# Performance work log

Hardware: AMD Instinct MI355X
Metric: run time of the kernel (lower is better)

## Reference

```python
import jax, jax.numpy as jnp
import numpy as np

N_HEADS = 16
B = 8
SEQ = 1024
HID = 1024
TOT = B * SEQ


def setup_inputs() -> dict:
    key = jax.random.key(0)
    k1, k2, k3 = jax.random.split(key, 3)
    hidden_states = jax.random.normal(k1, (TOT, HID), dtype=jnp.float32)
    Wqkv = jax.random.normal(k2, (3 * HID, HID), dtype=jnp.float32) * 0.02
    Bqkv = jax.random.normal(k3, (3 * HID,), dtype=jnp.float32) * 0.02
    cu_seqlens = (jnp.arange(B + 1, dtype=jnp.int32) * SEQ)
    return {"hidden_states": hidden_states, "Wqkv": Wqkv, "Bqkv": Bqkv,
            "cu_seqlens": cu_seqlens, "max_s": SEQ}


def reference(hidden_states, Wqkv, Bqkv, cu_seqlens, max_s):
    # qkv projection: F.linear(hidden, Wqkv, Bqkv) -> [T, 3H]
    T, H = hidden_states.shape
    h = N_HEADS
    d = H // h
    b = cu_seqlens.shape[0] - 1
    S = T // b  # equal-length packing; cu_seqlens = arange(b+1)*S
    qkv = hidden_states @ Wqkv.T + Bqkv                      # [T, 3H]
    qkv = qkv.reshape(b, S, 3, h, d)
    q, k, v = qkv[:, :, 0], qkv[:, :, 1], qkv[:, :, 2]       # [b, S, h, d]
    scale = 1.0 / jnp.sqrt(jnp.asarray(d, dtype=q.dtype))
    scores = jnp.einsum("bshd,bthd->bhst", q, k) * scale     # [b, h, S, S]
    probs = jax.nn.softmax(scores, axis=-1)                  # p_dropout = 0.0
    ctx = jnp.einsum("bhst,bthd->bshd", probs, v)            # [b, S, h, d]
    return ctx.reshape(T, H)
```

## Files before the change

### kernel.cpp

```cpp
#include <hip/hip_runtime.h>

typedef __attribute__((ext_vector_type(8))) __bf16 bf16x8;
typedef __attribute__((ext_vector_type(2))) __bf16 bf16x2;
typedef __attribute__((ext_vector_type(4))) float f32x4;
typedef __attribute__((ext_vector_type(4))) unsigned int u32x4;

#define AS1 __attribute__((address_space(1)))
#define AS3 __attribute__((address_space(3)))

__device__ __forceinline__ unsigned short f2b(float f) {
    union { float f; unsigned int u; } c; c.f = f;
    unsigned int r = c.u + 0x7fffu + ((c.u >> 16) & 1u);
    return (unsigned short)(r >> 16);
}

__device__ __forceinline__ unsigned int pack2(float a, float b) {
    bf16x2 t;
    t[0] = (__bf16)a;
    t[1] = (__bf16)b;
    return __builtin_bit_cast(unsigned int, t);
}

__device__ __forceinline__ void gload_lds16(const void* g, void* l) {
    __builtin_amdgcn_global_load_lds((const AS1 unsigned int*)g,
                                     (AS3 unsigned int*)l, 16, 0, 0);
}

__global__ void cvt2_kernel(const float* __restrict__ in0,
                            unsigned short* __restrict__ out0, int n0,
                            const float* __restrict__ in1,
                            unsigned short* __restrict__ out1, int n1) {
    int i = blockIdx.x * blockDim.x + threadIdx.x;
    int stride = gridDim.x * blockDim.x;
    const int nt = n0 + n1;
    for (; i < nt; i += stride) {
        if (i < n0) {
            float4 v = reinterpret_cast<const float4*>(in0)[i];
            ushort4 o;
            o.x = f2b(v.x); o.y = f2b(v.y); o.z = f2b(v.z); o.w = f2b(v.w);
            reinterpret_cast<ushort4*>(out0)[i] = o;
        } else {
            const int j = i - n0;
            const int E = j * 4;
            const int row = E >> 10;
            const int col = E & 1023;
            float4 v = reinterpret_cast<const float4*>(in1)[j];
            ushort4 o;
            o.x = f2b(v.x); o.y = f2b(v.y); o.z = f2b(v.z); o.w = f2b(v.w);
            const int kt = col >> 5, kg = (col >> 3) & 3, e = col & 7;
            const int n16 = row >> 4, fr = row & 15;
            const size_t oaddr = ((size_t)(kt * 192 + n16) << 9)
                               + ((kg * 16 + fr) << 3) + e;
            *reinterpret_cast<ushort4*>(out1 + oaddr) = o;
        }
    }
}

__global__ __launch_bounds__(512, 4) void qkv_gemm(
    const unsigned short* __restrict__ A,
    const unsigned short* __restrict__ Bw,
    const float* __restrict__ bias,
    unsigned short* __restrict__ qb,
    unsigned short* __restrict__ kb,
    unsigned short* __restrict__ vb)
{
    __shared__ __align__(16) char smem[49152];
    const int tid = threadIdx.x;
    const int lane = tid & 63, w = tid >> 6;
    const int wm = w >> 1, wn = w & 1;
    const int wg = (blockIdx.x & 7) * 96 + (blockIdx.x >> 3);
    const int mt = wg / 24;
    const int nt = wg % 24;
    const int fr = lane & 15, kg = lane >> 4;

    const int sr = lane >> 2;
    const int g  = (lane & 3) ^ ((sr >> 1) & 3);
    const unsigned short* a_srcg = A + (size_t)(mt * 256 + w * 16 + sr) * 1024 + g * 8;
    const unsigned short* bfp = Bw + (((size_t)(nt * 8 + wn * 4)) << 9) + lane * 8;

    f32x4 acc[4][4] = {};
    const int pg = (kg ^ ((fr >> 1) & 3)) * 16;
    const int aoffA = (wm * 64 + fr) * 64;

#define STAGE_FULL(buf, kt) do {                                    \
    char* Sb_ = smem + (buf) * 16384 + w * 1024;                    \
    const size_t ko_ = (size_t)(kt) * 32;                           \
    gload_lds16(a_srcg + ko_,          Sb_);                        \
    gload_lds16(a_srcg + 131072 + ko_, Sb_ + 8192);                 \
} while (0)

#define MM(m_, n_) do {                                                        \
    acc[m_][n_] = __builtin_amdgcn_mfma_f32_16x16x32_bf16(                     \
        af[m_], bf[n_], acc[m_][n_], 0, 0, 0);                                 \
} while (0)

#define GT(CUR, PRE, kt, DOSTAGE, WNSTR) do {                                  \
    const char* Ab_ = smem + (CUR) * 16384;                                    \
    char* Sb_ = smem + (PRE) * 16384 + w * 1024;                               \
    const size_t ko_ = (size_t)((kt) + 2) * 32;                                \
    const unsigned short* bq_ = bfp + (size_t)(kt) * 98304;                    \
    bf16x8 af[4], bf[4];                                                       \
    _Pragma("unroll")                                                          \
    for (int n = 0; n < 4; ++n)                                                \
        bf[n] = *reinterpret_cast<const bf16x8*>(bq_ + (n << 9));              \
    asm volatile("s_waitcnt vmcnt(" WNSTR ")" ::: "memory");                   \
    __builtin_amdgcn_s_barrier();                                              \
    _Pragma("unroll")                                                          \
    for (int m = 0; m < 4; ++m)                                                \
        af[m] = *reinterpret_cast<const bf16x8*>(Ab_ + aoffA + m * 1024 + pg); \
    if (DOSTAGE) {                                                             \
        gload_lds16(a_srcg + ko_,          Sb_);                               \
        gload_lds16(a_srcg + 131072 + ko_, Sb_ + 8192);                        \
    }                                                                          \
    __builtin_amdgcn_s_setprio(1);                                             \
    MM(0, 0); MM(1, 0); MM(2, 0); MM(3, 0);                                    \
    MM(0, 1); MM(1, 1); MM(2, 1); MM(3, 1);                                    \
    MM(0, 2); MM(1, 2); MM(2, 2); MM(3, 2);                                    \
    MM(0, 3); MM(1, 3); MM(2, 3); MM(3, 3);                                    \
    __builtin_amdgcn_s_setprio(0);                                             \
} while (0)

    STAGE_FULL(0, 0);
    STAGE_FULL(1, 1);
#pragma unroll 1
    for (int it = 0; it < 10; ++it) {
        const int t0 = it * 3;
        GT(0, 2, t0 + 0, 1, "6");
        GT(1, 0, t0 + 1, 1, "6");
        GT(2, 1, t0 + 2, 1, "6");
    }
    GT(0, 2, 30, 0, "6");
    GT(1, 0, 31, 0, "4");
    __syncthreads();

    const int sidx = nt >> 3;
    float bv[4];
#pragma unroll
    for (int n = 0; n < 4; ++n) bv[n] = bias[nt * 128 + wn * 64 + n * 16 + fr];

    unsigned short* Cs = (unsigned short*)smem;

    if (sidx < 2) {
        unsigned short* dstb = (sidx == 0) ? qb : kb;
        const float sc = (sidx == 0) ? 0.1803368801111f : 1.0f;
#pragma unroll
        for (int p = 0; p < 2; ++p) {
            if ((wm >> 1) == p) {
                const int r0 = (wm & 1) * 64;
#pragma unroll
                for (int m = 0; m < 4; ++m)
#pragma unroll
                    for (int n = 0; n < 4; ++n)
#pragma unroll
                        for (int r = 0; r < 4; ++r)
                            Cs[(r0 + m * 16 + kg * 4 + r) * 136 + wn * 64 + n * 16 + fr] =
                                f2b((acc[m][n][r] + bv[n]) * sc);
            }
            __syncthreads();
#pragma unroll
            for (int itc = 0; itc < 4; ++itc) {
                const int task = itc * 512 + tid;
                const int rl = task >> 4;
                const int i16 = task & 15;
                const int t = mt * 256 + p * 128 + rl;
                const int b_ = t >> 10, s = t & 1023;
                const int head = ((nt * 128 + i16 * 8) >> 6) & 15;
                u32x4 v = *reinterpret_cast<const u32x4*>(Cs + rl * 136 + i16 * 8);
                *reinterpret_cast<u32x4*>(
                    dstb + ((size_t)(b_ * 16 + head) * 1024 + s) * 64 + (i16 & 7) * 8) = v;
            }
            __syncthreads();
        }
    } else {
#pragma unroll
        for (int p = 0; p < 2; ++p) {
            if ((wm >> 1) == p) {
                const int r0 = (wm & 1) * 64;
#pragma unroll
                for (int m = 0; m < 4; ++m)
#pragma unroll
                    for (int n = 0; n < 4; ++n)
#pragma unroll
                        for (int j = 0; j < 2; ++j) {
                            unsigned int pk = pack2(acc[m][n][2 * j] + bv[n],
                                                    acc[m][n][2 * j + 1] + bv[n]);
                            *reinterpret_cast<unsigned int*>(
                                Cs + (wn * 64 + n * 16 + fr) * 136
                                   + r0 + m * 16 + kg * 4 + 2 * j) = pk;
                        }
            }
            __syncthreads();
#pragma unroll
            for (int itc = 0; itc < 4; ++itc) {
                const int task = itc * 512 + tid;
                const int c = task >> 4;
                const int i16 = task & 15;
                const int col = nt * 128 + c;
                const int head = (col >> 6) & 15;
                const int d = col & 63;
                const int b_ = (mt * 256) >> 10;
                const int s0 = (mt * 256 & 1023) + p * 128 + i16 * 8;
                u32x4 v = *reinterpret_cast<const u32x4*>(Cs + c * 136 + i16 * 8);
                *reinterpret_cast<u32x4*>(
                    vb + (size_t)((b_ * 16 + head) * 64 + d) * 1024 + s0) = v;
            }
            __syncthreads();
        }
    }
#undef STAGE_FULL
#undef GT
#undef MM
}

#define KVB 64
__global__ __launch_bounds__(256, 4) void attn_kernel(
    const unsigned short* __restrict__ qb,
    const unsigned short* __restrict__ kb,
    const unsigned short* __restrict__ vb,
    float* __restrict__ out)
{
    __shared__ __align__(16) char asmem[32768];
    const int tid = threadIdx.x;
    const int lane = tid & 63, w = tid >> 6;
    const int wg = (blockIdx.x & 7) * 128 + (blockIdx.x >> 3);
    const int bh = wg >> 3;
    const int qt = wg & 7;
    const int b_ = bh >> 4, h_ = bh & 15;
    const int fr = lane & 15, kg = lane >> 4;

    const unsigned short* qp = qb + ((size_t)bh * 1024 + qt * 128) * 64;
    const unsigned short* kp = kb + (size_t)bh * 1024 * 64;
    const unsigned short* vp = vb + (size_t)bh * 64 * 1024;

    bf16x8 qfr[2][2];
#pragma unroll
    for (int qf = 0; qf < 2; ++qf) {
        const unsigned short* qr = qp + (w * 32 + qf * 16 + fr) * 64 + kg * 8;
        qfr[qf][0] = *reinterpret_cast<const bf16x8*>(qr);
        qfr[qf][1] = *reinterpret_cast<const bf16x8*>(qr + 32);
    }

    float m_q[2] = {-1e30f, -1e30f}, l_q[2] = {0.f, 0.f};
    f32x4 o_acc[2][4] = {};

    const int ksr = w * 8 + (lane >> 3);
    const int kcb = (lane & 7) * 16;

#define ASTAGE(buf, kvt) do {                                                  \
    const int kv0_ = (kvt) * KVB;                                              \
    char* Kb_ = asmem + (buf) * 16384 + w * 1024;                              \
    char* Vb_ = Kb_ + 8192;                                                    \
    _Pragma("unroll")                                                          \
    for (int i = 0; i < 2; ++i) {                                              \
        const int st = i * 32 + ksr;                                           \
        const int key = ((st >> 5) << 5) | (((st & 15) >> 2) << 3)             \
                      | (((st >> 4) & 1) << 2) | (st & 3);                     \
        const int scb = kcb ^ ((st & 7) << 4);                                 \
        gload_lds16(kp + (size_t)(kv0_ + key) * 64 + (scb >> 1),               \
                    Kb_ + i * 4096);                                           \
        const int d_ = i * 32 + ksr;                                           \
        const int svb = kcb ^ ((d_ & 7) << 4);                                 \
        gload_lds16(vp + (size_t)d_ * 1024 + kv0_ + (svb >> 1),                \
                    Vb_ + i * 4096);                                           \
    }                                                                          \
} while (0)

#define ACOMP(buf) do {                                                        \
    const char* Kb = asmem + (buf) * 16384;                                    \
    const char* Vb = Kb + 8192;                                                \
    f32x4 sacc[2][4] = {};                                                     \
    __builtin_amdgcn_s_setprio(1);                                             \
    _Pragma("unroll")                                                          \
    for (int jt = 0; jt < 4; ++jt) {                                           \
        _Pragma("unroll")                                                      \
        for (int ks = 0; ks < 2; ++ks) {                                       \
            const int cb = (ks * 64 + kg * 16) ^ ((fr & 7) << 4);              \
            bf16x8 kf = *reinterpret_cast<const bf16x8*>(                      \
                Kb + (jt * 16 + fr) * 128 + cb);                               \
            _Pragma("unroll")                                                  \
            for (int qf = 0; qf < 2; ++qf)                                     \
                sacc[qf][jt] = __builtin_amdgcn_mfma_f32_16x16x32_bf16(        \
                    kf, qfr[qf][ks], sacc[qf][jt], 0, 0, 0);                   \
        }                                                                      \
    }                                                                          \
    __builtin_amdgcn_s_setprio(0);                                             \
    unsigned int P2[2][4][2];                                                  \
    _Pragma("unroll")                                                          \
    for (int qf = 0; qf < 2; ++qf) {                                           \
        float mx = -1e30f;                                                     \
        _Pragma("unroll")                                                      \
        for (int jt = 0; jt < 4; ++jt) {                                       \
            float a = fmaxf(fmaxf(sacc[qf][jt][0], sacc[qf][jt][1]),           \
                            fmaxf(sacc[qf][jt][2], sacc[qf][jt][3]));          \
            mx = fmaxf(mx, a);                                                 \
        }                                                                      \
        mx = fmaxf(mx, __shfl_xor(mx, 16, 64));                                \
        mx = fmaxf(mx, __shfl_xor(mx, 32, 64));                                \
        if (__any(mx > m_q[qf] + 8.0f)) {                                      \
            const float mn = fmaxf(m_q[qf], mx);                               \
            const float corr = __builtin_amdgcn_exp2f(m_q[qf] - mn);           \
            m_q[qf] = mn;                                                      \
            l_q[qf] *= corr;                                                   \
            float cr[4];                                                       \
            _Pragma("unroll")                                                  \
            for (int r = 0; r < 4; ++r)                                        \
                cr[r] = __shfl(corr, kg * 4 + r, 64);                          \
            _Pragma("unroll")                                                  \
            for (int d0 = 0; d0 < 4; ++d0)                                     \
                _Pragma("unroll")                                              \
                for (int r = 0; r < 4; ++r) o_acc[qf][d0][r] *= cr[r];         \
        }                                                                      \
        const float mn_ = m_q[qf];                                             \
        float rs = 0.f;                                                        \
        _Pragma("unroll")                                                      \
        for (int jt = 0; jt < 4; ++jt) {                                       \
            float p0 = __builtin_amdgcn_exp2f(sacc[qf][jt][0] - mn_);          \
            float p1 = __builtin_amdgcn_exp2f(sacc[qf][jt][1] - mn_);          \
            float p2 = __builtin_amdgcn_exp2f(sacc[qf][jt][2] - mn_);          \
            float p3 = __builtin_amdgcn_exp2f(sacc[qf][jt][3] - mn_);          \
            rs += (p0 + p1) + (p2 + p3);                                       \
            P2[qf][jt][0] = pack2(p0, p1);                                     \
            P2[qf][jt][1] = pack2(p2, p3);                                     \
        }                                                                      \
        rs += __shfl_xor(rs, 16, 64);                                          \
        rs += __shfl_xor(rs, 32, 64);                                          \
        l_q[qf] += rs;                                                         \
    }                                                                          \
    __builtin_amdgcn_s_setprio(1);                                             \
    _Pragma("unroll")                                                          \
    for (int c = 0; c < 2; ++c) {                                              \
        bf16x8 pa[2];                                                          \
        _Pragma("unroll")                                                      \
        for (int qf = 0; qf < 2; ++qf) {                                       \
            u32x4 pw = { P2[qf][2 * c][0], P2[qf][2 * c][1],                   \
                         P2[qf][2 * c + 1][0], P2[qf][2 * c + 1][1] };         \
            pa[qf] = __builtin_bit_cast(bf16x8, pw);                           \
        }                                                                      \
        _Pragma("unroll")                                                      \
        for (int d0 = 0; d0 < 4; ++d0) {                                       \
            const int dd = d0 * 16 + fr;                                       \
            const int cbv = (c * 64 + kg * 16) ^ ((dd & 7) << 4);              \
            bf16x8 vf = *reinterpret_cast<const bf16x8*>(Vb + dd * 128 + cbv); \
            _Pragma("unroll")                                                  \
            for (int qf = 0; qf < 2; ++qf)                                     \
                o_acc[qf][d0] = __builtin_amdgcn_mfma_f32_16x16x32_bf16(       \
                    pa[qf], vf, o_acc[qf][d0], 0, 0, 0);                       \
        }                                                                      \
    }                                                                          \
    __builtin_amdgcn_s_setprio(0);                                             \
} while (0)

    ASTAGE(0, 0);
#pragma unroll 1
    for (int t = 0; t < 15; ++t) {
        ASTAGE((t + 1) & 1, t + 1);
        asm volatile("s_waitcnt vmcnt(4) lgkmcnt(0)" ::: "memory");
        __builtin_amdgcn_s_barrier();
        ACOMP(t & 1);
        asm volatile("s_waitcnt lgkmcnt(0)" ::: "memory");
        __builtin_amdgcn_s_barrier();
    }
    asm volatile("s_waitcnt vmcnt(0) lgkmcnt(0)" ::: "memory");
    __builtin_amdgcn_s_barrier();
    ACOMP(1);

#pragma unroll
    for (int qf = 0; qf < 2; ++qf) {
        float linv[4];
#pragma unroll
        for (int r = 0; r < 4; ++r)
            linv[r] = 1.0f / __shfl(l_q[qf], kg * 4 + r, 64);
        const int trow = b_ * 1024 + qt * 128 + w * 32 + qf * 16;
#pragma unroll
        for (int d0 = 0; d0 < 4; ++d0) {
            const int c = h_ * 64 + d0 * 16 + fr;
#pragma unroll
            for (int r = 0; r < 4; ++r)
                out[(size_t)(trow + kg * 4 + r) * 1024 + c] = o_acc[qf][d0][r] * linv[r];
        }
    }
#undef ASTAGE
#undef ACOMP
}

extern "C" void kernel_launch(void* const* d_in, const int* in_sizes, int n_in,
                              void* d_out, int out_size, void* d_ws, size_t ws_size,
                              hipStream_t stream)
{
    const float* hs   = (const float*)d_in[0];
    const float* Wqkv = (const float*)d_in[1];
    const float* Bqkv = (const float*)d_in[2];
    float* out = (float*)d_out;

    char* ws = (char*)d_ws;
    unsigned short* hsb = (unsigned short*)(ws);
    unsigned short* wb  = (unsigned short*)(ws + (size_t)16 * 1048576);
    unsigned short* qb  = (unsigned short*)(ws + (size_t)22 * 1048576);
    unsigned short* kb  = (unsigned short*)(ws + (size_t)38 * 1048576);
    unsigned short* vb  = (unsigned short*)(ws + (size_t)54 * 1048576);

    cvt2_kernel<<<2048, 256, 0, stream>>>(hs, hsb, 8192 * 1024 / 4,
                                          Wqkv, wb, 3072 * 1024 / 4);
    qkv_gemm<<<768, 512, 0, stream>>>(hsb, wb, Bqkv, qb, kb, vb);
    attn_kernel<<<1024, 256, 0, stream>>>(qb, kb, vb, out);
}
```

Before: 147.7 us.

## Register double-buffer B fragments in QKV GEMM and coalesce weight conversion writes

The QKV GEMM now loads the next k-step's B fragments from global memory into a second register set one iteration ahead. The vmcnt wait and barrier move to the end of each step, so B-load latency overlaps the current MFMAs. The weight-conversion kernel is reorganized so each thread writes 8 contiguous output elements in packed order and reads gathered source rows, replacing the earlier scattered writes. Keeping two B fragment sets live raises register pressure and changes the wait counts.

```diff
diff --git a/kernel.cpp b/kernel.cpp
--- a/kernel.cpp
+++ b/kernel.cpp
@@ -40,18 +40,19 @@
             o.x = f2b(v.x); o.y = f2b(v.y); o.z = f2b(v.z); o.w = f2b(v.w);
             reinterpret_cast<ushort4*>(out0)[i] = o;
         } else {
-            const int j = i - n0;
-            const int E = j * 4;
-            const int row = E >> 10;
-            const int col = E & 1023;
-            float4 v = reinterpret_cast<const float4*>(in1)[j];
-            ushort4 o;
-            o.x = f2b(v.x); o.y = f2b(v.y); o.z = f2b(v.z); o.w = f2b(v.w);
-            const int kt = col >> 5, kg = (col >> 3) & 3, e = col & 7;
-            const int n16 = row >> 4, fr = row & 15;
-            const size_t oaddr = ((size_t)(kt * 192 + n16) << 9)
-                               + ((kg * 16 + fr) << 3) + e;
-            *reinterpret_cast<ushort4*>(out1 + oaddr) = o;
+            const int idx = i - n0;
+            const int blk = idx >> 6;
+            const int lane = idx & 63;
+            const int kt = blk / 192, n16 = blk % 192;
+            const int kg = lane >> 4, fr = lane & 15;
+            const size_t src = (size_t)(n16 * 16 + fr) * 1024 + kt * 32 + kg * 8;
+            float4 v0 = *reinterpret_cast<const float4*>(in1 + src);
+            float4 v1 = *reinterpret_cast<const float4*>(in1 + src + 4);
+            ushort4 o0, o1;
+            o0.x = f2b(v0.x); o0.y = f2b(v0.y); o0.z = f2b(v0.z); o0.w = f2b(v0.w);
+            o1.x = f2b(v1.x); o1.y = f2b(v1.y); o1.z = f2b(v1.z); o1.w = f2b(v1.w);
+            reinterpret_cast<ushort4*>(out1)[2 * idx]     = o0;
+            reinterpret_cast<ushort4*>(out1)[2 * idx + 1] = o1;
         }
     }
 }
@@ -82,6 +83,9 @@
     const int pg = (kg ^ ((fr >> 1) & 3)) * 16;
     const int aoffA = (wm * 64 + fr) * 64;
 
+    bf16x8 bfA0, bfA1, bfA2, bfA3;
+    bf16x8 bfB0, bfB1, bfB2, bfB3;
+
 #define STAGE_FULL(buf, kt) do {                                    \
     char* Sb_ = smem + (buf) * 16384 + w * 1024;                    \
     const size_t ko_ = (size_t)(kt) * 32;                           \
@@ -89,22 +93,32 @@
     gload_lds16(a_srcg + 131072 + ko_, Sb_ + 8192);                 \
 } while (0)
 
-#define MM(m_, n_) do {                                                        \
-    acc[m_][n_] = __builtin_amdgcn_mfma_f32_16x16x32_bf16(                     \
-        af[m_], bf[n_], acc[m_][n_], 0, 0, 0);                                 \
-} while (0)
-
-#define GT(CUR, PRE, kt, DOSTAGE, WNSTR) do {                                  \
+#define BLOAD(B0, B1, B2, B3, kt) do {                                         \
+    const unsigned short* bq_ = bfp + (size_t)(kt) * 98304;                    \
+    B0 = *reinterpret_cast<const bf16x8*>(bq_);                                \
+    B1 = *reinterpret_cast<const bf16x8*>(bq_ + 512);                          \
+    B2 = *reinterpret_cast<const bf16x8*>(bq_ + 1024);                         \
+    B3 = *reinterpret_cast<const bf16x8*>(bq_ + 1536);                         \
+} while (0)
+
+#define MMn(n_, BF_) do {                                                      \
+    acc[0][n_] = __builtin_amdgcn_mfma_f32_16x16x32_bf16(                      \
+        af[0], BF_, acc[0][n_], 0, 0, 0);                                      \
+    acc[1][n_] = __builtin_amdgcn_mfma_f32_16x16x32_bf16(                      \
+        af[1], BF_, acc[1][n_], 0, 0, 0);                                      \
+    acc[2][n_] = __builtin_amdgcn_mfma_f32_16x16x32_bf16(                      \
+        af[2], BF_, acc[2][n_], 0, 0, 0);                                      \
+    acc[3][n_] = __builtin_amdgcn_mfma_f32_16x16x32_bf16(                      \
+        af[3], BF_, acc[3][n_], 0, 0, 0);                                      \
+} while (0)
+
+#define GTN(CUR, PRE, kt, C0, C1, C2, C3, N0, N1, N2, N3, DOSTAGE, PF, WNSTR) \
+do {                                                                           \
     const char* Ab_ = smem + (CUR) * 16384;                                    \
     char* Sb_ = smem + (PRE) * 16384 + w * 1024;                               \
     const size_t ko_ = (size_t)((kt) + 2) * 32;                                \
-    const unsigned short* bq_ = bfp + (size_t)(kt) * 98304;                    \
-    bf16x8 af[4], bf[4];                                                       \
-    _Pragma("unroll")                                                          \
-    for (int n = 0; n < 4; ++n)                                                \
-        bf[n] = *reinterpret_cast<const bf16x8*>(bq_ + (n << 9));              \
-    asm volatile("s_waitcnt vmcnt(" WNSTR ")" ::: "memory");                   \
-    __builtin_amdgcn_s_barrier();                                              \
+    if (PF) BLOAD(N0, N1, N2, N3, (kt) + 1);                                   \
+    bf16x8 af[4];                                                              \
     _Pragma("unroll")                                                          \
     for (int m = 0; m < 4; ++m)                                                \
         af[m] = *reinterpret_cast<const bf16x8*>(Ab_ + aoffA + m * 1024 + pg); \
@@ -113,24 +127,29 @@
         gload_lds16(a_srcg + 131072 + ko_, Sb_ + 8192);                        \
     }                                                                          \
     __builtin_amdgcn_s_setprio(1);                                             \
-    MM(0, 0); MM(1, 0); MM(2, 0); MM(3, 0);                                    \
-    MM(0, 1); MM(1, 1); MM(2, 1); MM(3, 1);                                    \
-    MM(0, 2); MM(1, 2); MM(2, 2); MM(3, 2);                                    \
-    MM(0, 3); MM(1, 3); MM(2, 3); MM(3, 3);                                    \
+    MMn(0, C0); MMn(1, C1); MMn(2, C2); MMn(3, C3);                            \
     __builtin_amdgcn_s_setprio(0);                                             \
+    asm volatile("s_waitcnt vmcnt(" WNSTR ")" ::: "memory");                   \
+    __builtin_amdgcn_s_barrier();                                              \
 } while (0)
 
     STAGE_FULL(0, 0);
     STAGE_FULL(1, 1);
+    BLOAD(bfA0, bfA1, bfA2, bfA3, 0);
+    asm volatile("s_waitcnt vmcnt(6)" ::: "memory");
+    __builtin_amdgcn_s_barrier();
 #pragma unroll 1
-    for (int it = 0; it < 10; ++it) {
-        const int t0 = it * 3;
-        GT(0, 2, t0 + 0, 1, "6");
-        GT(1, 0, t0 + 1, 1, "6");
-        GT(2, 1, t0 + 2, 1, "6");
-    }
-    GT(0, 2, 30, 0, "6");
-    GT(1, 0, 31, 0, "4");
+    for (int it = 0; it < 5; ++it) {
+        const int t0 = it * 6;
+        GTN(0, 2, t0 + 0, bfA0, bfA1, bfA2, bfA3, bfB0, bfB1, bfB2, bfB3, 1, 1, "6");
+        GTN(1, 0, t0 + 1, bfB0, bfB1, bfB2, bfB3, bfA0, bfA1, bfA2, bfA3, 1, 1, "6");
+        GTN(2, 1, t0 + 2, bfA0, bfA1, bfA2, bfA3, bfB0, bfB1, bfB2, bfB3, 1, 1, "6");
+        GTN(0, 2, t0 + 3, bfB0, bfB1, bfB2, bfB3, bfA0, bfA1, bfA2, bfA3, 1, 1, "6");
+        GTN(1, 0, t0 + 4, bfA0, bfA1, bfA2, bfA3, bfB0, bfB1, bfB2, bfB3, 1, 1, "6");
+        GTN(2, 1, t0 + 5, bfB0, bfB1, bfB2, bfB3, bfA0, bfA1, bfA2, bfA3, 1, 1, "6");
+    }
+    GTN(0, 2, 30, bfA0, bfA1, bfA2, bfA3, bfB0, bfB1, bfB2, bfB3, 0, 1, "4");
+    GTN(1, 0, 31, bfB0, bfB1, bfB2, bfB3, bfA0, bfA1, bfA2, bfA3, 0, 0, "0");
     __syncthreads();
 
     const int sidx = nt >> 3;
@@ -208,8 +227,9 @@
         }
     }
 #undef STAGE_FULL
-#undef GT
-#undef MM
+#undef BLOAD
+#undef MMn
+#undef GTN
 }
 
 #define KVB 64
@@ -400,7 +420,7 @@
     unsigned short* vb  = (unsigned short*)(ws + (size_t)54 * 1048576);
 
     cvt2_kernel<<<2048, 256, 0, stream>>>(hs, hsb, 8192 * 1024 / 4,
-                                          Wqkv, wb, 3072 * 1024 / 4);
+                                          Wqkv, wb, 3072 * 1024 / 8);
     qkv_gemm<<<768, 512, 0, stream>>>(hsb, wb, Bqkv, qb, kb, vb);
     attn_kernel<<<1024, 256, 0, stream>>>(qb, kb, vb, out);
 }
```

Result: faster. 127.0 us (-14.0%).
